# Kernel tuning notes

Measured on AMD Instinct MI355X. Metric: run time of the kernel, lower is better.

The kernel has to match this reference:

```python
import jax, jax.numpy as jnp
import numpy as np

B, N, D, K = 64, 4096, 256, 32


def setup_inputs() -> dict:
    key = jax.random.key(0)
    kx, kc, ks = jax.random.split(key, 3)
    x = jax.random.normal(kx, (B, N, D), dtype=jnp.float32)
    # codebook: 'orthogonal' init approximated by normalized gaussian rows
    C = jax.random.normal(kc, (K, D), dtype=jnp.float32) / np.sqrt(D)
    # keras 'uniform' initializer: U(-0.05, 0.05)
    S = jax.random.uniform(ks, (K,), dtype=jnp.float32, minval=-0.05, maxval=0.05)
    return {"x": x, "C": C, "S": S}


def reference(x, C, S):
    """Deep-TEN encoding.
    r_ik = x_i - C_k ;  w = softmax_k(-S_k * ||r_ik||^2) ;  E_k = sum_i w_ik * r_ik.
    ||r||^2 expanded as ||x||^2 - 2 x.C + ||C||^2 to avoid the [B,N,K,D] residual;
    aggregation likewise split: E = einsum(w, x) - (sum_i w) * C.
    """
    x2 = jnp.sum(x * x, axis=-1, keepdims=True)          # [B,N,1]
    c2 = jnp.sum(C * C, axis=-1)                         # [K]
    xc = jnp.einsum('bnd,kd->bnk', x, C)                 # [B,N,K]
    dist = x2 - 2.0 * xc + c2                            # [B,N,K] = ||x_i - C_k||^2
    w = jax.nn.softmax(-S * dist, axis=-1)               # [B,N,K]
    # E_k = sum_i w_ik * (x_i - C_k)
    E = jnp.einsum('bnk,bnd->bkd', w, x) - jnp.sum(w, axis=1)[..., None] * C
    return E                                             # [B,K,D]
```

## Files before the change

kernel.cpp:

```cpp
#include <hip/hip_runtime.h>
#include <stdint.h>


#define NN 4096
#define DD 256
#define KK 32
#define WTP 72

typedef __attribute__((ext_vector_type(8))) short short8;
typedef __attribute__((ext_vector_type(4))) float float4v;

__device__ __forceinline__ unsigned pk2t(float a, float b) {
    return __builtin_amdgcn_perm(__float_as_uint(b), __float_as_uint(a), 0x07060302u);
}
__device__ __forceinline__ unsigned short f2bf_rne(float f) {
    unsigned u = __float_as_uint(f);
    return (unsigned short)((u + 0x7fffu + ((u >> 16) & 1u)) >> 16);
}
__device__ __forceinline__ short8 pack8_rne(float4 a, float4 b) {
    short8 r;
    r[0] = (short)f2bf_rne(a.x); r[1] = (short)f2bf_rne(a.y);
    r[2] = (short)f2bf_rne(a.z); r[3] = (short)f2bf_rne(a.w);
    r[4] = (short)f2bf_rne(b.x); r[5] = (short)f2bf_rne(b.y);
    r[6] = (short)f2bf_rne(b.z); r[7] = (short)f2bf_rne(b.w);
    return r;
}
__device__ __forceinline__ int swx(int n) { return (n & 7) ^ ((n >> 2) & 6); }
__device__ __forceinline__ int gfun(int l) { return (l & 15) ^ (l >> 4); }

#define DPP_ADD(v, ctrl) \
    ((v) + __int_as_float(__builtin_amdgcn_update_dpp( \
        0, __float_as_int(v), (ctrl), 0xf, 0xf, true)))

__launch_bounds__(256, 2)
__global__ void dten_kernel(const float* __restrict__ X,
                            const float* __restrict__ Cg,
                            const float* __restrict__ Sg,
                            float* __restrict__ ws) {
    const int b     = blockIdx.y;
    const int chunk = blockIdx.x;
    const int tid   = threadIdx.x;
    const int lane  = tid & 63;
    const int wv    = tid >> 6;
    const int lk    = lane & 15;
    const int lq    = lane >> 4;

    __shared__ __align__(16) unsigned short xa[64 * 256];
    __shared__ __align__(16) unsigned xt32[256 * 32];
    __shared__ __align__(16) unsigned short wt[KK * WTP];
    __shared__ __align__(16) float x2s[64];
    __shared__ __align__(16) float c2p[8][32];
    __shared__ __align__(16) float c2s[32];
    __shared__ __align__(16) float wss[4][32];

    {
        int k = tid & 31, seg = tid >> 5;
        const float4* cr = (const float4*)(Cg + k * DD + seg * 32);
        float p = 0.f;
        #pragma unroll
        for (int i = 0; i < 8; ++i) {
            float4 u = cr[i];
            p += u.x*u.x + u.y*u.y + u.z*u.z + u.w*u.w;
        }
        c2p[seg][k] = p;
    }
    __syncthreads();
    if (tid < 32) {
        float s = 0.f;
        #pragma unroll
        for (int seg = 0; seg < 8; ++seg) s += c2p[seg][tid];
        c2s[tid] = s;
    }
    __syncthreads();

    float sk8[8], c2k8[8];
    #pragma unroll
    for (int kt = 0; kt < 2; ++kt)
        #pragma unroll
        for (int r = 0; r < 4; ++r) {
            int k = 16 * kt + 4 * lq + r;
            sk8[kt * 4 + r]  = Sg[k];
            c2k8[kt * 4 + r] = c2s[k];
        }

    short8 cfrag[2][8];
    #pragma unroll
    for (int kt = 0; kt < 2; ++kt) {
        const float* crow = Cg + (size_t)(16 * kt + lk) * DD + lq * 8;
        #pragma unroll
        for (int ch = 0; ch < 8; ++ch) {
            float4 u0 = *(const float4*)(crow + ch * 32);
            float4 u1 = *(const float4*)(crow + ch * 32 + 4);
            cfrag[kt][ch] = pack8_rne(u0, u1);
        }
    }

    float4v eacc[2][4];
    #pragma unroll
    for (int i = 0; i < 2; ++i)
        #pragma unroll
        for (int j = 0; j < 4; ++j)
            eacc[i][j] = (float4v){0.f, 0.f, 0.f, 0.f};
    float wsr[8] = {0.f, 0.f, 0.f, 0.f, 0.f, 0.f, 0.f, 0.f};

    const int row_base = chunk * 256;
    const int nown = 16 * wv + lk;
    const int glane = gfun(lane);

    for (int t = 0; t < 4; ++t) {
        const int row0 = row_base + t * 64;
        __syncthreads();

        const float4* xt4 = (const float4*)(X + ((size_t)b * NN + row0) * DD);
        #pragma unroll
        for (int it = 0; it < 8; ++it) {
            const int P  = 8 * wv + it;
            const int r0 = 2 * P, r1 = r0 + 1;
            float4 v0 = xt4[r0 * 64 + lane];
            float4 v1 = xt4[r1 * 64 + lane];
            float p0 = v0.x*v0.x + v0.y*v0.y + v0.z*v0.z + v0.w*v0.w;
            float p1 = v1.x*v1.x + v1.y*v1.y + v1.z*v1.z + v1.w*v1.w;
            p0 = DPP_ADD(p0, 0x111); p1 = DPP_ADD(p1, 0x111);
            p0 = DPP_ADD(p0, 0x112); p1 = DPP_ADD(p1, 0x112);
            p0 = DPP_ADD(p0, 0x114); p1 = DPP_ADD(p1, 0x114);
            p0 = DPP_ADD(p0, 0x118); p1 = DPP_ADD(p1, 0x118);
            p0 = DPP_ADD(p0, 0x142); p1 = DPP_ADD(p1, 0x142);
            p0 = DPP_ADD(p0, 0x143); p1 = DPP_ADD(p1, 0x143);
            if (lane == 63) { x2s[r0] = p0; x2s[r1] = p1; }
            {
                int cs0 = (lane >> 1) ^ swx(r0);
                int cs1 = (lane >> 1) ^ swx(r1);
                *(uint2*)&xa[r0 * 256 + cs0 * 8 + 4 * (lane & 1)] =
                    make_uint2(pk2t(v0.x, v0.y), pk2t(v0.z, v0.w));
                *(uint2*)&xa[r1 * 256 + cs1 * 8 + 4 * (lane & 1)] =
                    make_uint2(pk2t(v1.x, v1.y), pk2t(v1.z, v1.w));
            }
            {
                int base = lane * 128 + (P ^ glane);
                xt32[base     ] = pk2t(v0.x, v1.x);
                xt32[base + 32] = pk2t(v0.y, v1.y);
                xt32[base + 64] = pk2t(v0.z, v1.z);
                xt32[base + 96] = pk2t(v0.w, v1.w);
            }
        }

        float4v a0 = (float4v){0.f, 0.f, 0.f, 0.f};
        float4v a1 = (float4v){0.f, 0.f, 0.f, 0.f};
        {
            const int rowoff = nown * 256;
            const int s = swx(nown);
            #pragma unroll
            for (int ch = 0; ch < 8; ++ch) {
                int c = (4 * ch + lq) ^ s;
                short8 bf = *(const short8*)&xa[rowoff + c * 8];
                a0 = __builtin_amdgcn_mfma_f32_16x16x32_bf16(cfrag[0][ch], bf, a0, 0, 0, 0);
                a1 = __builtin_amdgcn_mfma_f32_16x16x32_bf16(cfrag[1][ch], bf, a1, 0, 0, 0);
            }
        }
        float x2n = x2s[nown];
        float aa[8];
        #pragma unroll
        for (int r = 0; r < 4; ++r) {
            aa[r]     = sk8[r]     * (2.f * a0[r] - x2n - c2k8[r]);
            aa[4 + r] = sk8[4 + r] * (2.f * a1[r] - x2n - c2k8[4 + r]);
        }
        float m = aa[0];
        #pragma unroll
        for (int i = 1; i < 8; ++i) m = fmaxf(m, aa[i]);
        m = fmaxf(m, __shfl_xor(m, 16));
        m = fmaxf(m, __shfl_xor(m, 32));
        float e[8], den = 0.f;
        #pragma unroll
        for (int i = 0; i < 8; ++i) { e[i] = __expf(aa[i] - m); den += e[i]; }
        den += __shfl_xor(den, 16);
        den += __shfl_xor(den, 32);
        float inv = __builtin_amdgcn_rcpf(den);
        #pragma unroll
        for (int i = 0; i < 8; ++i) {
            float w = e[i] * inv;
            wsr[i] += w;
            int k = 16 * (i >> 2) + 4 * lq + (i & 3);
            wt[k * WTP + nown] = (unsigned short)(__float_as_uint(w) >> 16);
        }
        __syncthreads();

        #pragma unroll
        for (int s = 0; s < 2; ++s) {
            short8 af0 = *(const short8*)&wt[lk * WTP + s * 32 + lq * 8];
            short8 af1 = *(const short8*)&wt[(16 + lk) * WTP + s * 32 + lq * 8];
            #pragma unroll
            for (int dt = 0; dt < 4; ++dt) {
                const int d  = 64 * wv + 16 * dt + lk;
                const int gl = gfun(d >> 2);
                const int bb = d * 32 + s * 16;
                short8 bf;
                unsigned* bw = (unsigned*)&bf;
                bw[0] = xt32[bb + ((4 * lq + 0) ^ gl)];
                bw[1] = xt32[bb + ((4 * lq + 1) ^ gl)];
                bw[2] = xt32[bb + ((4 * lq + 2) ^ gl)];
                bw[3] = xt32[bb + ((4 * lq + 3) ^ gl)];
                eacc[0][dt] = __builtin_amdgcn_mfma_f32_16x16x32_bf16(af0, bf, eacc[0][dt], 0, 0, 0);
                eacc[1][dt] = __builtin_amdgcn_mfma_f32_16x16x32_bf16(af1, bf, eacc[1][dt], 0, 0, 0);
            }
        }
    }

    #pragma unroll
    for (int i = 0; i < 8; ++i) {
        wsr[i] += __shfl_xor(wsr[i], 1);
        wsr[i] += __shfl_xor(wsr[i], 2);
        wsr[i] += __shfl_xor(wsr[i], 4);
        wsr[i] += __shfl_xor(wsr[i], 8);
    }
    if (lk == 0) {
        #pragma unroll
        for (int i = 0; i < 8; ++i) {
            int k = 16 * (i >> 2) + 4 * lq + (i & 3);
            wss[wv][k] = wsr[i];
        }
    }
    __syncthreads();

    float* wsp = ws + (((size_t)b * 16 + chunk) * KK) * DD;
    #pragma unroll
    for (int kt = 0; kt < 2; ++kt) {
        #pragma unroll
        for (int r = 0; r < 4; ++r) {
            int k = 16 * kt + 4 * lq + r;
            float wsk = wss[0][k] + wss[1][k] + wss[2][k] + wss[3][k];
            #pragma unroll
            for (int dt = 0; dt < 4; ++dt) {
                int d = 64 * wv + 16 * dt + lk;
                wsp[k * DD + d] = eacc[kt][dt][r] - wsk * Cg[(size_t)k * DD + d];
            }
        }
    }
}

__launch_bounds__(256)
__global__ void reduce_kernel(const float* __restrict__ ws,
                              float* __restrict__ out) {
    const int o = blockIdx.x * 256 + threadIdx.x;
    const int b = o >> 11;
    const int rest = o & 2047;
    const float4* w4 = (const float4*)ws + ((size_t)b * 16) * 2048 + rest;
    float4 acc = make_float4(0.f, 0.f, 0.f, 0.f);
    #pragma unroll
    for (int c = 0; c < 16; ++c) {
        float4 v = w4[(size_t)c * 2048];
        acc.x += v.x; acc.y += v.y; acc.z += v.z; acc.w += v.w;
    }
    ((float4*)out)[o] = acc;
}

extern "C" void kernel_launch(void* const* d_in, const int* in_sizes, int n_in,
                              void* d_out, int out_size, void* d_ws, size_t ws_size,
                              hipStream_t stream) {
    const float* X = (const float*)d_in[0];
    const float* C = (const float*)d_in[1];
    const float* S = (const float*)d_in[2];
    float* out = (float*)d_out;
    float* ws  = (float*)d_ws;
    dim3 grid(16, 64);
    dten_kernel<<<grid, dim3(256), 0, stream>>>(X, C, S, ws);
    reduce_kernel<<<dim3(512), dim3(256), 0, stream>>>(ws, out);
}
```

Before: 386.6 us.

## Drop transposed LDS copy of x and gather B fragments from row-major tile

Removes the separate transposed bf16 copy of the x tile (xt32, 32 KB of LDS) and instead builds the aggregation MFMA B operand by gathering eight 16-bit elements per lane from the existing swizzled row-major tile. This cuts LDS use so the launch bound can be raised from 2 to 4 blocks per CU, and it drops the transpose stores. The trade is more, narrower LDS reads (8 ushort loads per fragment instead of 4 dword loads) with possible bank conflicts, plus tighter register limits that may cause spills. WTP padding is also changed.

```diff
diff --git a/kernel.cpp b/kernel.cpp
--- a/kernel.cpp
+++ b/kernel.cpp
@@ -5,7 +5,7 @@
 #define NN 4096
 #define DD 256
 #define KK 32
-#define WTP 72
+#define WTP 80
 
 typedef __attribute__((ext_vector_type(8))) short short8;
 typedef __attribute__((ext_vector_type(4))) float float4v;
@@ -26,13 +26,12 @@
     return r;
 }
 __device__ __forceinline__ int swx(int n) { return (n & 7) ^ ((n >> 2) & 6); }
-__device__ __forceinline__ int gfun(int l) { return (l & 15) ^ (l >> 4); }
 
 #define DPP_ADD(v, ctrl) \
     ((v) + __int_as_float(__builtin_amdgcn_update_dpp( \
         0, __float_as_int(v), (ctrl), 0xf, 0xf, true)))
 
-__launch_bounds__(256, 2)
+__launch_bounds__(256, 4)
 __global__ void dten_kernel(const float* __restrict__ X,
                             const float* __restrict__ Cg,
                             const float* __restrict__ Sg,
@@ -46,7 +45,6 @@
     const int lq    = lane >> 4;
 
     __shared__ __align__(16) unsigned short xa[64 * 256];
-    __shared__ __align__(16) unsigned xt32[256 * 32];
     __shared__ __align__(16) unsigned short wt[KK * WTP];
     __shared__ __align__(16) float x2s[64];
     __shared__ __align__(16) float c2p[8][32];
@@ -105,7 +103,6 @@
 
     const int row_base = chunk * 256;
     const int nown = 16 * wv + lk;
-    const int glane = gfun(lane);
 
     for (int t = 0; t < 4; ++t) {
         const int row0 = row_base + t * 64;
@@ -127,21 +124,12 @@
             p0 = DPP_ADD(p0, 0x142); p1 = DPP_ADD(p1, 0x142);
             p0 = DPP_ADD(p0, 0x143); p1 = DPP_ADD(p1, 0x143);
             if (lane == 63) { x2s[r0] = p0; x2s[r1] = p1; }
-            {
-                int cs0 = (lane >> 1) ^ swx(r0);
-                int cs1 = (lane >> 1) ^ swx(r1);
-                *(uint2*)&xa[r0 * 256 + cs0 * 8 + 4 * (lane & 1)] =
-                    make_uint2(pk2t(v0.x, v0.y), pk2t(v0.z, v0.w));
-                *(uint2*)&xa[r1 * 256 + cs1 * 8 + 4 * (lane & 1)] =
-                    make_uint2(pk2t(v1.x, v1.y), pk2t(v1.z, v1.w));
-            }
-            {
-                int base = lane * 128 + (P ^ glane);
-                xt32[base     ] = pk2t(v0.x, v1.x);
-                xt32[base + 32] = pk2t(v0.y, v1.y);
-                xt32[base + 64] = pk2t(v0.z, v1.z);
-                xt32[base + 96] = pk2t(v0.w, v1.w);
-            }
+            int cs0 = (lane >> 1) ^ swx(r0);
+            int cs1 = (lane >> 1) ^ swx(r1);
+            *(uint2*)&xa[r0 * 256 + cs0 * 8 + 4 * (lane & 1)] =
+                make_uint2(pk2t(v0.x, v0.y), pk2t(v0.z, v0.w));
+            *(uint2*)&xa[r1 * 256 + cs1 * 8 + 4 * (lane & 1)] =
+                make_uint2(pk2t(v1.x, v1.y), pk2t(v1.z, v1.w));
         }
 
         float4v a0 = (float4v){0.f, 0.f, 0.f, 0.f};
@@ -185,20 +173,18 @@
         __syncthreads();
 
         #pragma unroll
-        for (int s = 0; s < 2; ++s) {
-            short8 af0 = *(const short8*)&wt[lk * WTP + s * 32 + lq * 8];
-            short8 af1 = *(const short8*)&wt[(16 + lk) * WTP + s * 32 + lq * 8];
+        for (int nc = 0; nc < 2; ++nc) {
+            short8 af0 = *(const short8*)&wt[lk * WTP + nc * 32 + lq * 8];
+            short8 af1 = *(const short8*)&wt[(16 + lk) * WTP + nc * 32 + lq * 8];
             #pragma unroll
             for (int dt = 0; dt < 4; ++dt) {
-                const int d  = 64 * wv + 16 * dt + lk;
-                const int gl = gfun(d >> 2);
-                const int bb = d * 32 + s * 16;
+                const int cb = 8 * wv + 2 * dt + (lk >> 3);
                 short8 bf;
-                unsigned* bw = (unsigned*)&bf;
-                bw[0] = xt32[bb + ((4 * lq + 0) ^ gl)];
-                bw[1] = xt32[bb + ((4 * lq + 1) ^ gl)];
-                bw[2] = xt32[bb + ((4 * lq + 2) ^ gl)];
-                bw[3] = xt32[bb + ((4 * lq + 3) ^ gl)];
+                #pragma unroll
+                for (int j = 0; j < 8; ++j) {
+                    int n2 = nc * 32 + lq * 8 + j;
+                    bf[j] = (short)xa[n2 * 256 + ((cb ^ swx(n2)) << 3) + (lk & 7)];
+                }
                 eacc[0][dt] = __builtin_amdgcn_mfma_f32_16x16x32_bf16(af0, bf, eacc[0][dt], 0, 0, 0);
                 eacc[1][dt] = __builtin_amdgcn_mfma_f32_16x16x32_bf16(af1, bf, eacc[1][dt], 0, 0, 0);
             }
```

After: 457.8 us. 1.18x slower.
